# Performance work log

Hardware: AMD Instinct MI355X
Metric: run time of the kernel (lower is better)

## Reference

```python
import jax, jax.numpy as jnp
import numpy as np

NUM_EMBEDDINGS = 512
EMBEDDING_DIM = 64
BETA = 0.25


def setup_inputs() -> dict:
    key = jax.random.key(0)
    k1, k2 = jax.random.split(key)
    latent_z = jax.random.normal(k1, (32, EMBEDDING_DIM, 64, 64), dtype=jnp.float32)
    # nn.Embedding init: uniform(-1/K, 1/K)
    scale = 1.0 / NUM_EMBEDDINGS
    embedding = jax.random.uniform(k2, (NUM_EMBEDDINGS, EMBEDDING_DIM), dtype=jnp.float32,
                                   minval=-scale, maxval=scale)
    return {"latent_z": latent_z, "embedding": embedding}


def reference(latent_z, embedding):
    # [B, C, H, W] -> [B, H, W, C]
    z = jnp.transpose(latent_z, (0, 2, 3, 1))
    B, H, W, D = z.shape
    flat_z = z.reshape(-1, D)  # [N, D]

    # squared L2 distances via expansion: ||z||^2 + ||e||^2 - 2 z.e
    dist = (jnp.sum(flat_z ** 2, axis=1, keepdims=True)
            + jnp.sum(embedding ** 2, axis=1)
            - 2.0 * flat_z @ embedding.T)  # [N, K]

    idx = jnp.argmin(dist, axis=1)  # [N]
    encodings = jax.nn.one_hot(idx, NUM_EMBEDDINGS, dtype=flat_z.dtype)  # [N, K]

    # gather codes (same math as one_hot @ embedding)
    quantized = embedding[idx].reshape(B, H, W, D)

    quant_loss = (jnp.mean((jax.lax.stop_gradient(quantized) - z) ** 2)
                  + BETA * jnp.mean((quantized - jax.lax.stop_gradient(z)) ** 2))

    # straight-through estimator
    quantized_st = z + jax.lax.stop_gradient(quantized - z)

    mean_enc = jnp.mean(encodings, axis=0)
    perplexity = jnp.exp(-jnp.sum(mean_enc * jnp.log(mean_enc + 1e-10)))

    quantized_out = jnp.transpose(quantized_st, (0, 3, 1, 2))  # back to [B, C, H, W]
    return quant_loss, quantized_out, perplexity, encodings, idx[:, None]
```

## Files before the change

### kernel.cpp

```cpp
#include <hip/hip_runtime.h>
#include <math.h>

#define NPIX   131072
#define KCODES 512
#define DIM    64
#define HW     4096
#define CHW    262144
#define NBLK   1024

#define O_Q    1ll
#define O_PERP 8388609ll
#define O_ENC  8388610ll
#define O_IDX  75497474ll

#define WS_EMBT 1280

#define GLD16(gp, lp) __builtin_amdgcn_global_load_lds( \
    (const __attribute__((address_space(1))) unsigned int*)(gp), \
    (__attribute__((address_space(3))) unsigned int*)(lp), 16, 0, 0)

__device__ __forceinline__ float np_sumsq64(const float (&x)[64]) {
#pragma clang fp contract(off)
  float r0 = x[0]*x[0], r1 = x[1]*x[1], r2 = x[2]*x[2], r3 = x[3]*x[3];
  float r4 = x[4]*x[4], r5 = x[5]*x[5], r6 = x[6]*x[6], r7 = x[7]*x[7];
#pragma unroll
  for (int i = 8; i < 64; i += 8) {
    r0 += x[i+0]*x[i+0];
    r1 += x[i+1]*x[i+1];
    r2 += x[i+2]*x[i+2];
    r3 += x[i+3]*x[i+3];
    r4 += x[i+4]*x[i+4];
    r5 += x[i+5]*x[i+5];
    r6 += x[i+6]*x[i+6];
    r7 += x[i+7]*x[i+7];
  }
  return ((r0+r1)+(r2+r3))+((r4+r5)+(r6+r7));
}

__global__ void vq_prep(const float* __restrict__ emb, float* __restrict__ ws) {
  const int t = threadIdx.x;
  if (t == 0) ws[0] = 0.0f;
  ((unsigned*)ws)[1 + t] = 0u;
  float x[64];
  const float* e = emb + t * DIM;
#pragma unroll
  for (int d = 0; d < 64; ++d) x[d] = e[d];
  ws[513 + t] = np_sumsq64(x);
#pragma unroll
  for (int d = 0; d < 64; ++d) ws[WS_EMBT + d * 512 + t] = x[d];
}


__device__ __forceinline__ void issue_ET(const float* __restrict__ embT,
                                         float* __restrict__ dstbuf,
                                         int g, int wv, int lane) {
#pragma unroll
  for (int q = 0; q < 2; ++q) {
    const int r = 2 * wv + q;
    const float* gp = embT + (size_t)((g & 3) * 16 + r) * 512
                    + 256 * (g >> 2) + 4 * lane;
    GLD16(gp, dstbuf + r * 256);
  }
}

__device__ __forceinline__ void enc_zero(float2* __restrict__ encb, int g, int t) {
  const float2 zz = make_float2(0.0f, 0.0f);
#pragma unroll
  for (int u = 0; u < 8; ++u)
    encb[(size_t)g * 4096 + u * 512 + t] = zz;
}

__device__ __forceinline__ void dl_loop(const float* __restrict__ ETb,
                                        const float* __restrict__ zl,
                                        int sdim, int pi, int ci,
                                        float (&acc)[8][8]) {
#pragma unroll 2
  for (int dl = 0; dl < 16; ++dl) {
    const float* zp = &zl[(sdim + dl) * 128 + 8 * pi];
    const float4 za0 = *(const float4*)(zp + 0);
    const float4 za1 = *(const float4*)(zp + 4);
    const float* ep = &ETb[dl * 256 + 4 * ci];
    const float4 e0 = *(const float4*)(ep + 0);
    const float4 e1 = *(const float4*)(ep + 128);
    const float zr[8] = {za0.x, za0.y, za0.z, za0.w,
                         za1.x, za1.y, za1.z, za1.w};
    const float er_[8] = {e0.x, e0.y, e0.z, e0.w,
                          e1.x, e1.y, e1.z, e1.w};
#pragma unroll
    for (int j = 0; j < 8; ++j)
#pragma unroll
      for (int c = 0; c < 8; ++c)
        acc[j][c] = fmaf(zr[j], er_[c], acc[j][c]);
  }
}

__device__ __forceinline__ void dist_phase(int Hh, int ci, int pi,
                                           const float (&acc)[8][8],
                                           const float* __restrict__ esq_l,
                                           const float* __restrict__ zsq_l,
                                           float (&bd)[8], int (&bk)[8]) {
#pragma unroll
  for (int q = 0; q < 2; ++q)
#pragma unroll
    for (int r = 0; r < 4; ++r) {
      const int k = 256 * Hh + 128 * q + 4 * ci + r;
      const float eq = esq_l[k];
#pragma unroll
      for (int j = 0; j < 8; ++j) {
        const float dist = (zsq_l[8 * pi + j] + eq) - 2.0f * acc[j][4 * q + r];
        if (dist < bd[j]) { bd[j] = dist; bk[j] = k; }
      }
    }
}

__global__ __launch_bounds__(512, 4)
void vq_main(
    const float* __restrict__ z, const float* __restrict__ emb,
    float* __restrict__ out, float* __restrict__ ws)
{
  __shared__ float ET_s[2][16 * 256];
  __shared__ float z_l[64 * 128];
  __shared__ float esq_l[512];
  __shared__ float zsq_l[128];
  __shared__ int   ridx_l[128];
  __shared__ float wsum[8];

  const int t    = threadIdx.x;
  const int lane = t & 63;
  const int wv   = t >> 6;
  const int ci   = t & 31;
  const int pi   = t >> 5;
  const int blk  = blockIdx.x;
  const int n0   = blk * 128;
  const int b    = n0 >> 12;
  const int hw0  = n0 & 4095;
  const float* zg   = z + (size_t)b * CHW + hw0;
  const float* embT = ws + WS_EMBT;

  esq_l[t] = ws[513 + t];

#pragma unroll
  for (int c = 0; c < 4; ++c) {
    const int d0 = 2 * (4 * wv + c);
    const float* gp = zg + (size_t)(d0 + (lane >> 5)) * HW + 4 * (lane & 31);
    GLD16(gp, &z_l[d0 * 128]);
  }

  issue_ET(embT, &ET_s[0][0], 0, wv, lane);

  __syncthreads();

  if (t < 128) {
    float x[64];
#pragma unroll
    for (int d = 0; d < 64; ++d) x[d] = z_l[d * 128 + t];
    zsq_l[t] = np_sumsq64(x);
  }

  float bd[8];
  int   bk[8];
#pragma unroll
  for (int j = 0; j < 8; ++j) { bd[j] = INFINITY; bk[j] = 0; }
  float acc[8][8];
#pragma unroll
  for (int j = 0; j < 8; ++j)
#pragma unroll
    for (int c = 0; c < 8; ++c) acc[j][c] = 0.0f;

  float2* encb = (float2*)(out + O_ENC) + (size_t)n0 * 256;

  for (int g = 0; g < 8; ++g) {
    if (g < 7) issue_ET(embT, &ET_s[(g + 1) & 1][0], g + 1, wv, lane);
    enc_zero(encb, g, t);
    __builtin_amdgcn_s_setprio(1);
    dl_loop(&ET_s[g & 1][0], z_l, 16 * (g & 3), pi, ci, acc);
    __builtin_amdgcn_s_setprio(0);
    if ((g & 3) == 3) {
      dist_phase(g >> 2, ci, pi, acc, esq_l, zsq_l, bd, bk);
      if (g == 3) {
#pragma unroll
        for (int j = 0; j < 8; ++j)
#pragma unroll
          for (int c = 0; c < 8; ++c) acc[j][c] = 0.0f;
      }
    }
    __syncthreads();
  }

#pragma unroll
  for (int m = 16; m >= 1; m >>= 1) {
#pragma unroll
    for (int j = 0; j < 8; ++j) {
      const float od = __shfl_xor(bd[j], m, 64);
      const int   ok = __shfl_xor(bk[j], m, 64);
      if (od < bd[j] || (od == bd[j] && ok < bk[j])) { bd[j] = od; bk[j] = ok; }
    }
  }
  if (ci == 0) {
#pragma unroll
    for (int j = 0; j < 8; ++j) ridx_l[8 * pi + j] = bk[j];
  }
  __syncthreads();

  if (t < 128) {
    const int k = ridx_l[t];
    out[O_IDX + n0 + t] = (float)k;
    atomicAdd((unsigned*)ws + 1 + k, 1u);
    out[O_ENC + (size_t)(n0 + t) * 512 + k] = 1.0f;
  }

  {
    const int px = t & 127;
    const int dq = t >> 7;
    const int k  = ridx_l[px];
    const float* e0 = emb + ((size_t)k << 6);
    float* q0 = out + O_Q + (size_t)b * CHW + hw0 + px;
    float lsum = 0.0f;
#pragma unroll
    for (int j = 0; j < 16; ++j) {
      const int d = dq * 16 + j;
      const float ev = e0[d];
      const float df = ev - z_l[d * 128 + px];
      lsum = fmaf(df, df, lsum);
      q0[(size_t)d * HW] = ev;
    }
#pragma unroll
    for (int off = 32; off > 0; off >>= 1) lsum += __shfl_down(lsum, off, 64);
    if ((t & 63) == 0) wsum[t >> 6] = lsum;
  }
  __syncthreads();
  if (t == 0)
    atomicAdd(ws, ((wsum[0] + wsum[1]) + (wsum[2] + wsum[3])) +
                  ((wsum[4] + wsum[5]) + (wsum[6] + wsum[7])));
}

__global__ void vq_fin(float* __restrict__ out, const float* __restrict__ ws) {
  __shared__ float red[8];
  const int t = threadIdx.x;
  const unsigned* counts = (const unsigned*)ws + 1;
  const float p = (float)counts[t] * (1.0f / 131072.0f);
  float h = p * logf(p + 1e-10f);
#pragma unroll
  for (int off = 32; off > 0; off >>= 1) h += __shfl_down(h, off, 64);
  if ((t & 63) == 0) red[t >> 6] = h;
  __syncthreads();
  if (t == 0) {
    float H = 0.0f;
#pragma unroll
    for (int w = 0; w < 8; ++w) H += red[w];
    out[O_PERP] = expf(-H);
    out[0] = 1.25f * ws[0] * (1.0f / 8388608.0f);
  }
}

extern "C" void kernel_launch(void* const* d_in, const int* in_sizes, int n_in,
                              void* d_out, int out_size, void* d_ws, size_t ws_size,
                              hipStream_t stream) {
  const float* z   = (const float*)d_in[0];
  const float* emb = (const float*)d_in[1];
  float* out = (float*)d_out;
  float* ws  = (float*)d_ws;

  vq_prep<<<1, 512, 0, stream>>>(emb, ws);
  vq_main<<<NBLK, 512, 0, stream>>>(z, emb, out, ws);
  vq_fin<<<1, 512, 0, stream>>>(out, ws);
}
```

Measured before the change: 433.5 us.

## Split one-hot and quantized output writes into a separate write kernel

```diff
diff --git a/kernel.cpp b/kernel.cpp
--- a/kernel.cpp
+++ b/kernel.cpp
@@ -61,13 +61,6 @@
                     + 256 * (g >> 2) + 4 * lane;
     GLD16(gp, dstbuf + r * 256);
   }
-}
-
-__device__ __forceinline__ void enc_zero(float2* __restrict__ encb, int g, int t) {
-  const float2 zz = make_float2(0.0f, 0.0f);
-#pragma unroll
-  for (int u = 0; u < 8; ++u)
-    encb[(size_t)g * 4096 + u * 512 + t] = zz;
 }
 
 __device__ __forceinline__ void dl_loop(const float* __restrict__ ETb,
@@ -167,11 +160,8 @@
 #pragma unroll
     for (int c = 0; c < 8; ++c) acc[j][c] = 0.0f;
 
-  float2* encb = (float2*)(out + O_ENC) + (size_t)n0 * 256;
-
   for (int g = 0; g < 8; ++g) {
     if (g < 7) issue_ET(embT, &ET_s[(g + 1) & 1][0], g + 1, wv, lane);
-    enc_zero(encb, g, t);
     __builtin_amdgcn_s_setprio(1);
     dl_loop(&ET_s[g & 1][0], z_l, 16 * (g & 3), pi, ci, acc);
     __builtin_amdgcn_s_setprio(0);
@@ -206,7 +196,6 @@
     const int k = ridx_l[t];
     out[O_IDX + n0 + t] = (float)k;
     atomicAdd((unsigned*)ws + 1 + k, 1u);
-    out[O_ENC + (size_t)(n0 + t) * 512 + k] = 1.0f;
   }
 
   {
@@ -214,15 +203,12 @@
     const int dq = t >> 7;
     const int k  = ridx_l[px];
     const float* e0 = emb + ((size_t)k << 6);
-    float* q0 = out + O_Q + (size_t)b * CHW + hw0 + px;
     float lsum = 0.0f;
 #pragma unroll
     for (int j = 0; j < 16; ++j) {
       const int d = dq * 16 + j;
-      const float ev = e0[d];
-      const float df = ev - z_l[d * 128 + px];
+      const float df = e0[d] - z_l[d * 128 + px];
       lsum = fmaf(df, df, lsum);
-      q0[(size_t)d * HW] = ev;
     }
 #pragma unroll
     for (int off = 32; off > 0; off >>= 1) lsum += __shfl_down(lsum, off, 64);
@@ -232,6 +218,40 @@
   if (t == 0)
     atomicAdd(ws, ((wsum[0] + wsum[1]) + (wsum[2] + wsum[3])) +
                   ((wsum[4] + wsum[5]) + (wsum[6] + wsum[7])));
+}
+
+__global__ __launch_bounds__(256, 8)
+void vq_write(const float* __restrict__ emb, float* __restrict__ out) {
+  __shared__ int idx_l[256];
+  const int t  = threadIdx.x;
+  const int p0 = blockIdx.x * 256;
+
+  idx_l[t] = (int)out[O_IDX + p0 + t];
+  __syncthreads();
+
+  float2* enc = (float2*)(out + O_ENC) + (size_t)p0 * 256;
+#pragma unroll 8
+  for (int row = 0; row < 256; ++row) {
+    const int k = idx_l[row];
+    float2 v = make_float2(0.0f, 0.0f);
+    if ((k >> 1) == t) { if (k & 1) v.y = 1.0f; else v.x = 1.0f; }
+    enc[(size_t)row * 256 + t] = v;
+  }
+
+  {
+    const int b = p0 >> 12, hw0 = p0 & 4095;
+    const int k = idx_l[t];
+    const float* e0 = emb + ((size_t)k << 6);
+    float* q0 = out + O_Q + (size_t)b * CHW + hw0 + t;
+#pragma unroll
+    for (int dv = 0; dv < 16; ++dv) {
+      const float4 ev = *(const float4*)(e0 + 4 * dv);
+      q0[(size_t)(4 * dv + 0) * HW] = ev.x;
+      q0[(size_t)(4 * dv + 1) * HW] = ev.y;
+      q0[(size_t)(4 * dv + 2) * HW] = ev.z;
+      q0[(size_t)(4 * dv + 3) * HW] = ev.w;
+    }
+  }
 }
 
 __global__ void vq_fin(float* __restrict__ out, const float* __restrict__ ws) {
@@ -263,5 +283,6 @@
 
   vq_prep<<<1, 512, 0, stream>>>(emb, ws);
   vq_main<<<NBLK, 512, 0, stream>>>(z, emb, out, ws);
+  vq_write<<<NPIX / 256, 256, 0, stream>>>(emb, out);
   vq_fin<<<1, 512, 0, stream>>>(out, ws);
 }
```

After: 461.9 us. +6.6%, slower.
